# Optimization experiments

Hardware: AMD Instinct MI355X
Metric: run time of the kernel (lower is better)

## Reference

```python
import jax, jax.numpy as jnp
import numpy as np

N_SAMPLES = 32768
N_ATOMS = 1024
ATOM_LEN = 2048
N_TO_KEEP = 1024


def fft_convolve(a, b):
    """Linear convolution via FFT: zero-pad both to 2n, multiply spectra, truncate to n."""
    n = a.shape[-1]
    a = jnp.pad(a, [(0, 0)] * (a.ndim - 1) + [(0, n)])
    b = jnp.pad(b, [(0, 0)] * (b.ndim - 1) + [(0, n)])
    spec = jnp.fft.rfft(a, axis=-1) * jnp.fft.rfft(b, axis=-1)  # broadcast (B,1024,2n//2+1)
    return jnp.fft.irfft(spec, axis=-1)[..., :n]


def sparsify(x, n_to_keep):
    """Keep the top-k raw values over the flattened per-batch feature map; zero the rest."""
    shp = x.shape
    flat = x.reshape(shp[0], -1)                       # (B, 1024*32768)
    vals, idx = jax.lax.top_k(flat, n_to_keep)         # (B, k)
    out = jnp.zeros_like(flat).at[jnp.arange(shp[0])[:, None], idx].set(vals)
    return out.reshape(shp)


def setup_inputs() -> dict:
    key = jax.random.key(0)
    k1, k2 = jax.random.split(key)
    x = jax.random.normal(k1, (2, 1, N_SAMPLES), dtype=jnp.float32)
    # atoms initialized uniform(-0.01, 0.01) in the original module
    atoms = jax.random.uniform(k2, (1, N_ATOMS, ATOM_LEN), dtype=jnp.float32,
                               minval=-0.01, maxval=0.01)
    return {"x": x, "atoms": atoms}


def reference(x, atoms):
    padded = jnp.pad(atoms, ((0, 0), (0, 0), (0, N_SAMPLES - atoms.shape[-1])))  # (1,1024,32768)
    fm = fft_convolve(x, padded)            # (B, 1024, 32768)
    fm = sparsify(fm, N_TO_KEEP)
    recon = fft_convolve(fm, padded)        # (B, 1024, 32768)
    recon = jnp.sum(recon, axis=1, keepdims=True)  # (B, 1, 32768)
    return recon
```

## Files before the change

### kernel.cpp

```cpp
#include <hip/hip_runtime.h>
#include <hip/hip_bf16.h>

#define NS    32768
#define NA    1024
#define AL    2048
#define KKEEP 1024
#define CAPC  (512*1024)

struct Cand { float v; unsigned idx; };

typedef short  short8  __attribute__((ext_vector_type(8)));
typedef short  short4v __attribute__((ext_vector_type(4)));
typedef float  f32x4   __attribute__((ext_vector_type(4)));


__device__ inline unsigned short f2bf(float f) {
    union { float f; unsigned u; } v; v.f = f;
    unsigned r = v.u + 0x7fffu + ((v.u >> 16) & 1u);
    return (unsigned short)(r >> 16);
}

__global__ void prep_kernel(const float* __restrict__ x, const float* __restrict__ atoms,
                            float* __restrict__ psum, unsigned* __restrict__ candCnt,
                            unsigned short* __restrict__ ab16) {
    __shared__ float red[12];
    const int bid = blockIdx.x;
    const int tid = threadIdx.x;
    const int i   = bid * 256 + tid;
    float4 f = *(const float4*)(atoms + (size_t)i * 4);
    ushort4 o;
    o.x = f2bf(f.x); o.y = f2bf(f.y); o.z = f2bf(f.z); o.w = f2bf(f.w);
    *(ushort4*)(ab16 + (size_t)i * 4) = o;
    float sa  = f.x*f.x + f.y*f.y + f.z*f.z + f.w*f.w;
    float sx0 = 0.f, sx1 = 0.f;
    if (i < 16384) {
        float4 xv = *(const float4*)(x + (size_t)i * 4);
        float s = xv.x*xv.x + xv.y*xv.y + xv.z*xv.z + xv.w*xv.w;
        if (i < 8192) sx0 = s; else sx1 = s;
    }
    #pragma unroll
    for (int off = 32; off >= 1; off >>= 1) {
        sa  += __shfl_down(sa , off);
        sx0 += __shfl_down(sx0, off);
        sx1 += __shfl_down(sx1, off);
    }
    if ((tid & 63) == 0) {
        red[(tid >> 6) * 3 + 0] = sa;
        red[(tid >> 6) * 3 + 1] = sx0;
        red[(tid >> 6) * 3 + 2] = sx1;
    }
    __syncthreads();
    if (tid == 0) {
        psum[bid * 3 + 0] = red[0] + red[3] + red[6] + red[9];
        psum[bid * 3 + 1] = red[1] + red[4] + red[7] + red[10];
        psum[bid * 3 + 2] = red[2] + red[5] + red[8] + red[11];
        if (bid == 0) { candCnt[0] = 0u; candCnt[1] = 0u; }
    }
}

#define XRW      2175
#define XRSTRIDE 2192
#define XRB      4384
#define NCPY     4
#define SA_BUF   16384

__device__ inline void gload_lds16(const unsigned short* g, unsigned char* lds) {
    __builtin_amdgcn_global_load_lds((const __attribute__((address_space(1))) void*)g,
                                     (__attribute__((address_space(3))) void*)lds,
                                     16, 0, 0);
}

__global__ __launch_bounds__(256, 3)
void fm_kernel(const float* __restrict__ x, const float* __restrict__ af32,
               const unsigned short* __restrict__ ab16,
               const float* __restrict__ psum, unsigned* __restrict__ candCnt,
               Cand* __restrict__ cand, unsigned cap)
{
    __shared__ __align__(16) unsigned char  sA[2 * SA_BUF];
    __shared__ __align__(16) unsigned short sXR[NCPY * XRSTRIDE];
    __shared__ float    sred[12];
    __shared__ double   sredd[4];
    __shared__ unsigned bq_pos[64];
    __shared__ unsigned bq_idx[64];
    __shared__ int      bq_n;

    const int bid = blockIdx.x;
    const int b   = bid >> 11;
    const int rem = bid & 2047;
    const int a0  = (rem >> 8) * 128;
    const int t0  = (rem & 255) * 128;

    const int tid  = threadIdx.x;
    const int lane = tid & 63;
    const int wid  = tid >> 6;
    const int wm   = wid >> 1;
    const int wn   = wid & 1;
    const int g    = lane >> 4;
    const int ln   = lane & 15;

    const int rot = (bid * 5) & 31;

    const float* __restrict__ xb = x + b * NS;

    for (int ti = tid; ti < XRW; ti += 256) {
        int t = t0 - 2047 + ti;
        float f = (t >= 0) ? xb[t] : 0.f;
        unsigned short h = f2bf(f);
        int p0 = 2174 - ti;
        #pragma unroll
        for (int m = 0; m < NCPY; ++m) sXR[m * XRSTRIDE + p0 + m] = h;
    }

    if (tid == 0) bq_n = 0;
    {
        float pa = 0.f, p0s = 0.f, p1s = 0.f;
        for (int j = tid; j < 2048; j += 256) {
            pa  += psum[3 * j + 0];
            p0s += psum[3 * j + 1];
            p1s += psum[3 * j + 2];
        }
        #pragma unroll
        for (int o = 32; o >= 1; o >>= 1) {
            pa  += __shfl_down(pa , o);
            p0s += __shfl_down(p0s, o);
            p1s += __shfl_down(p1s, o);
        }
        if ((tid & 63) == 0) {
            sred[(tid >> 6) * 3 + 0] = pa;
            sred[(tid >> 6) * 3 + 1] = p0s;
            sred[(tid >> 6) * 3 + 2] = p1s;
        }
    }

    #define STAGE(bf, ck) do {                                                   \
        int kcs = (ck) * 64;                                                     \
        _Pragma("unroll")                                                        \
        for (int it = 0; it < 4; ++it) {                                         \
            int slot = (wid * 4 + it) * 64 + lane;                               \
            int row  = slot >> 3;                                                \
            int blk  = slot & 7;                                                 \
            const unsigned short* gsrc =                                         \
                ab16 + (size_t)(a0 + row) * AL + kcs + ((blk ^ (row & 7)) << 3); \
            gload_lds16(gsrc, sA + (bf) * SA_BUF + (size_t)(wid * 4 + it) * 1024); \
        }                                                                        \
    } while (0)

    f32x4 acc[4][4];
    #pragma unroll
    for (int i = 0; i < 4; ++i)
        #pragma unroll
        for (int j = 0; j < 4; ++j) acc[i][j] = (f32x4)0.0f;

    const int Rbase = 127 - wn * 64 - ln + 8 * g;
    const unsigned char* xrb = (const unsigned char*)sXR;

    int rowoff[4];
    #pragma unroll
    for (int mi = 0; mi < 4; ++mi) rowoff[mi] = (wm * 64 + mi * 16 + ln) * 128;
    const int swz0 = ((0 * 4 + g) ^ (ln & 7)) << 4;
    const int swz1 = ((1 * 4 + g) ^ (ln & 7)) << 4;

    #define LOADB(Rv, dst) do {                                                 \
        int p_ = ((Rv) + 3) & ~3;                                               \
        const unsigned char* a_ =                                               \
            xrb + (unsigned)(p_ - (Rv)) * XRB + (unsigned)p_ * 2u;              \
        short4v lo_ = *(const short4v*)a_;                                      \
        short4v hi_ = *(const short4v*)(a_ + 8);                                \
        dst = __builtin_shufflevector(lo_, hi_, 0, 1, 2, 3, 4, 5, 6, 7);        \
    } while (0)

    short8 b0, b1, b2, b3;

    #define LOADB4(Sv) do {                        \
        LOADB(Rbase      + 32 * (Sv), b0);         \
        LOADB(Rbase - 16 + 32 * (Sv), b1);         \
        LOADB(Rbase - 32 + 32 * (Sv), b2);         \
        LOADB(Rbase - 48 + 32 * (Sv), b3);         \
    } while (0)

    #define ROLLB(Sv) do {                         \
        b3 = b1; b2 = b0;                          \
        LOADB(Rbase      + 32 * (Sv), b0);         \
        LOADB(Rbase - 16 + 32 * (Sv), b1);         \
    } while (0)

    #define MFMAS(mi) do {                                                                  \
        acc[mi][0] = __builtin_amdgcn_mfma_f32_16x16x32_bf16(af[mi], b0, acc[mi][0],0,0,0); \
        acc[mi][1] = __builtin_amdgcn_mfma_f32_16x16x32_bf16(af[mi], b1, acc[mi][1],0,0,0); \
        acc[mi][2] = __builtin_amdgcn_mfma_f32_16x16x32_bf16(af[mi], b2, acc[mi][2],0,0,0); \
        acc[mi][3] = __builtin_amdgcn_mfma_f32_16x16x32_bf16(af[mi], b3, acc[mi][3],0,0,0); \
    } while (0)

    __syncthreads();

    const float SAs = sred[0] + sred[3] + sred[6] + sred[9];
    const float S0s = sred[1] + sred[4] + sred[7] + sred[10];
    const float S1s = sred[2] + sred[5] + sred[8] + sred[11];
    const float sig = sqrtf((SAs * (1.0f / (float)NA)) *
                            (((b == 0) ? S0s : S1s) * (1.0f / (float)NS)));
    const float T0 = 3.70f * sig;
    const float TB = 3.85f * sig;

    LOADB4(rot * 2);

    STAGE(0, rot);
    STAGE(1, (rot + 1) & 31);

    for (int c = 0; c < 32; ++c) {
        const int chunk  = (c + rot) & 31;
        const int nchunk = (c + 1 + rot) & 31;
        const int cur    = c & 1;

        asm volatile("s_waitcnt vmcnt(4)" ::: "memory");
        __builtin_amdgcn_sched_barrier(0);
        __builtin_amdgcn_s_barrier();
        __builtin_amdgcn_sched_barrier(0);

        #pragma unroll
        for (int s = 0; s < 2; ++s) {
            short8 af[4];
            const int soff = cur * SA_BUF + (s ? swz1 : swz0);
            #pragma unroll
            for (int mi = 0; mi < 4; ++mi)
                af[mi] = *(const short8*)(sA + soff + rowoff[mi]);

            __builtin_amdgcn_s_setprio(1);
            MFMAS(0); MFMAS(1); MFMAS(2); MFMAS(3);
            __builtin_amdgcn_s_setprio(0);

            if (s == 0) {
                ROLLB(chunk * 2 + 1);
            } else {
                if (nchunk == 0) { LOADB4(0); }
                else             { ROLLB(nchunk * 2); }
            }
        }

        __builtin_amdgcn_sched_barrier(0);
        __builtin_amdgcn_s_barrier();
        __builtin_amdgcn_sched_barrier(0);

        STAGE(cur, (c + 2 + rot) & 31);
    }
    #undef LOADB
    #undef LOADB4
    #undef ROLLB
    #undef MFMAS
    #undef STAGE

    #pragma unroll
    for (int mi = 0; mi < 4; ++mi) {
        #pragma unroll
        for (int ni = 0; ni < 4; ++ni) {
            #pragma unroll
            for (int r = 0; r < 4; ++r) {
                float v = acc[mi][ni][r];
                if (v > T0) {
                    unsigned a = (unsigned)(a0 + wm * 64 + mi * 16 + g * 4 + r);
                    unsigned t = (unsigned)(t0 + wn * 64 + ni * 16 + ln);
                    unsigned idx = (a << 15) | t;
                    unsigned pos = atomicAdd(&candCnt[b], 1u);
                    if (pos < cap) {
                        Cand cc; cc.v = v; cc.idx = idx;
                        cand[(size_t)b * cap + pos] = cc;
                        if (v > TB) {
                            int q = atomicAdd(&bq_n, 1);
                            if (q < 64) { bq_pos[q] = pos; bq_idx[q] = idx; }
                        }
                    }
                }
            }
        }
    }
    __syncthreads();

    int nq = bq_n; if (nq > 64) nq = 64;
    for (int e = 0; e < nq; ++e) {
        const unsigned ie = bq_idx[e];
        const unsigned pe = bq_pos[e];
        const int aa = (int)(ie >> 15);
        const int tt = (int)(ie & (NS - 1));
        const float* __restrict__ ar = af32 + (size_t)aa * AL;
        double s = 0.0;
        #pragma unroll
        for (int kk = 0; kk < 8; ++kk) {
            int k = tid + kk * 256;
            int xi = tt - k;
            if (xi >= 0) s += (double)ar[k] * (double)xb[xi];
        }
        #pragma unroll
        for (int o = 32; o >= 1; o >>= 1) s += __shfl_down(s, o);
        if (lane == 0) sredd[wid] = s;
        __syncthreads();
        if (tid == 0)
            cand[(size_t)b * cap + pe].v =
                (float)(sredd[0] + sredd[1] + sredd[2] + sredd[3]);
        __syncthreads();
    }
}

#define SELCAP 16384

__global__ void select_kernel(const unsigned* __restrict__ candCnt,
                              const Cand* __restrict__ cand, Cand* __restrict__ sel,
                              unsigned cap) {
    __shared__ float    s_vals[SELCAP];
    __shared__ float    s_red[16];
    __shared__ int      s_cnt;
    __shared__ int      s_nA;
    __shared__ int      s_nT;
    __shared__ int      s_exact;
    __shared__ float    s_tau;
    __shared__ Cand     s_A[KKEEP];
    __shared__ unsigned s_T[256];

    const int b = blockIdx.x;
    const Cand* __restrict__ cb = cand + (size_t)b * cap;
    const int n   = (int)min(candCnt[b], cap);
    const int tid = threadIdx.x;

    if (n <= KKEEP) {
        for (int i = tid; i < KKEEP; i += blockDim.x) {
            Cand z; z.v = 0.f; z.idx = 0u;
            sel[b * KKEEP + i] = (i < n) ? cb[i] : z;
        }
        return;
    }

    const bool useLds = (n <= SELCAP);
    if (useLds)
        for (int i = tid; i < n; i += blockDim.x) s_vals[i] = cb[i].v;

    float m = 0.f;
    if (useLds) { __syncthreads();
        for (int i = tid; i < n; i += blockDim.x) m = fmaxf(m, s_vals[i]);
    } else {
        for (int i = tid; i < n; i += blockDim.x) m = fmaxf(m, cb[i].v);
    }
    #pragma unroll
    for (int o = 32; o >= 1; o >>= 1) m = fmaxf(m, __shfl_down(m, o));
    if ((tid & 63) == 0) s_red[tid >> 6] = m;
    if (tid == 0) s_exact = 0;
    __syncthreads();
    float hi;
    {
        float mm = 0.f;
        #pragma unroll
        for (int w = 0; w < 16; ++w) mm = fmaxf(mm, s_red[w]);
        hi = mm;
    }
    float lo = 0.f;
    for (int iter = 0; iter < 64; ++iter) {
        float mid = 0.5f * (lo + hi);
        if (!(mid > lo && mid < hi)) break;
        if (tid == 0) s_cnt = 0;
        __syncthreads();
        int c = 0;
        if (useLds) for (int i = tid; i < n; i += blockDim.x) c += (s_vals[i] > mid) ? 1 : 0;
        else        for (int i = tid; i < n; i += blockDim.x) c += (cb[i].v  > mid) ? 1 : 0;
        #pragma unroll
        for (int o = 32; o >= 1; o >>= 1) c += __shfl_down(c, o);
        if ((tid & 63) == 0) atomicAdd(&s_cnt, c);
        __syncthreads();
        int cm = s_cnt;
        __syncthreads();
        if (cm == KKEEP) { if (tid == 0) { s_tau = mid; s_exact = 1; } break; }
        if (cm > KKEEP) lo = mid; else hi = mid;
    }
    __syncthreads();

    const int   exact = s_exact;
    const float tau   = exact ? s_tau : hi;

    for (int i = tid; i < KKEEP; i += blockDim.x) { s_A[i].v = 0.f; s_A[i].idx = 0u; }
    if (tid == 0) { s_nA = 0; s_nT = 0; }
    __syncthreads();

    for (int i = tid; i < n; i += blockDim.x) {
        float v = cb[i].v;
        if (v > tau) {
            int p = atomicAdd(&s_nA, 1);
            if (p < KKEEP) s_A[p] = cb[i];
        } else if (!exact && v == tau) {
            int p = atomicAdd(&s_nT, 1);
            if (p < 256) s_T[p] = cb[i].idx;
        }
    }
    __syncthreads();
    if (tid == 0) {
        int nA = s_nA; if (nA > KKEEP) nA = KKEEP;
        int need = KKEEP - nA;
        int nT = s_nT; if (nT > 256) nT = 256;
        for (int r = 0; r < need && r < nT; ++r) {
            unsigned best = 0xffffffffu; int bj = -1;
            for (int j = 0; j < nT; ++j) if (s_T[j] < best) { best = s_T[j]; bj = j; }
            Cand c; c.v = tau; c.idx = best;
            s_A[nA + r] = c;
            if (bj >= 0) s_T[bj] = 0xffffffffu;
        }
    }
    __syncthreads();
    for (int i = tid; i < KKEEP; i += blockDim.x) sel[b * KKEEP + i] = s_A[i];
}

__global__ void recon_kernel(const float* __restrict__ atoms, const Cand* __restrict__ sel,
                             float* __restrict__ out) {
    __shared__ float s_cv[KKEEP];
    __shared__ int   s_ca[KKEEP];
    __shared__ int   s_ct[KKEEP];
    __shared__ int   s_n;
    const int b    = blockIdx.x >> 7;
    const int tseg = (blockIdx.x & 127) << 8;
    const int t    = tseg + threadIdx.x;
    if (threadIdx.x == 0) s_n = 0;
    __syncthreads();
    for (int i = threadIdx.x; i < KKEEP; i += blockDim.x) {
        Cand c = sel[b * KKEEP + i];
        int t0e = (int)(c.idx & (NS - 1));
        if (c.v != 0.f && t0e <= tseg + 255 && t0e + (AL - 1) >= tseg) {
            int p = atomicAdd(&s_n, 1);
            s_cv[p] = c.v;
            s_ca[p] = (int)(c.idx >> 15);
            s_ct[p] = t0e;
        }
    }
    __syncthreads();
    const int n = s_n;
    float acc = 0.f;
    for (int e = 0; e < n; ++e) {
        int d = t - s_ct[e];
        if ((unsigned)d < (unsigned)AL)
            acc += s_cv[e] * atoms[(size_t)s_ca[e] * AL + d];
    }
    out[b * NS + t] = acc;
}

extern "C" void kernel_launch(void* const* d_in, const int* in_sizes, int n_in,
                              void* d_out, int out_size, void* d_ws, size_t ws_size,
                              hipStream_t stream) {
    const float* x     = (const float*)d_in[0];
    const float* atoms = (const float*)d_in[1];
    float* out = (float*)d_out;

    unsigned*       candCnt = (unsigned*)d_ws;
    float*          psum    = (float*)((char*)d_ws + 64);
    Cand*           sel     = (Cand*)((char*)d_ws + 32768);
    unsigned short* ab16    = (unsigned short*)((char*)d_ws + 65536);
    const size_t    candOff = 65536 + (size_t)NA * AL * 2;
    Cand*           cand    = (Cand*)((char*)d_ws + candOff);

    unsigned cap = CAPC;
    if (ws_size > candOff + 2 * sizeof(Cand) * 1024) {
        size_t fit = (ws_size - candOff) / (2 * sizeof(Cand));
        if (fit < cap) cap = (unsigned)fit;
    } else {
        cap = 1024;
    }

    prep_kernel  <<<2048, 256, 0, stream>>>(x, atoms, psum, candCnt, ab16);
    fm_kernel    <<<2 * (NA / 128) * (NS / 128), 256, 0, stream>>>(x, atoms, ab16, psum, candCnt, cand, cap);
    select_kernel<<<2, 1024, 0, stream>>>(candCnt, cand, sel, cap);
    recon_kernel <<<256, 256, 0, stream>>>(atoms, sel, out);
}
```

Measured before the change: 420.4 us.

## Move fp64 band refinement out of fm_kernel into separate wave-per-candidate kernel

The exact fp64 recomputation of borderline candidates (value above a higher band threshold) is taken out of the GEMM-style fm_kernel, where it ran serially per block with two block barriers per candidate. A new refine_band kernel scans all candidates after fm_kernel, and one wavefront refines each candidate above the band threshold. This removes tail latency and LDS from the hot kernel, which may help occupancy, and spreads the refinement across the whole GPU. The cost is an extra launch and a full re-read of the candidate list. The 64-per-block cap on refined candidates is also gone.

```diff
diff --git a/kernel.cpp b/kernel.cpp
--- a/kernel.cpp
+++ b/kernel.cpp
@@ -71,18 +71,14 @@
 }
 
 __global__ __launch_bounds__(256, 3)
-void fm_kernel(const float* __restrict__ x, const float* __restrict__ af32,
+void fm_kernel(const float* __restrict__ x,
                const unsigned short* __restrict__ ab16,
                const float* __restrict__ psum, unsigned* __restrict__ candCnt,
                Cand* __restrict__ cand, unsigned cap)
 {
     __shared__ __align__(16) unsigned char  sA[2 * SA_BUF];
     __shared__ __align__(16) unsigned short sXR[NCPY * XRSTRIDE];
-    __shared__ float    sred[12];
-    __shared__ double   sredd[4];
-    __shared__ unsigned bq_pos[64];
-    __shared__ unsigned bq_idx[64];
-    __shared__ int      bq_n;
+    __shared__ float sred[12];
 
     const int bid = blockIdx.x;
     const int b   = bid >> 11;
@@ -111,7 +107,6 @@
         for (int m = 0; m < NCPY; ++m) sXR[m * XRSTRIDE + p0 + m] = h;
     }
 
-    if (tid == 0) bq_n = 0;
     {
         float pa = 0.f, p0s = 0.f, p1s = 0.f;
         for (int j = tid; j < 2048; j += 256) {
@@ -199,7 +194,6 @@
     const float sig = sqrtf((SAs * (1.0f / (float)NA)) *
                             (((b == 0) ? S0s : S1s) * (1.0f / (float)NS)));
     const float T0 = 3.70f * sig;
-    const float TB = 3.85f * sig;
 
     LOADB4(rot * 2);
 
@@ -263,39 +257,70 @@
                     if (pos < cap) {
                         Cand cc; cc.v = v; cc.idx = idx;
                         cand[(size_t)b * cap + pos] = cc;
-                        if (v > TB) {
-                            int q = atomicAdd(&bq_n, 1);
-                            if (q < 64) { bq_pos[q] = pos; bq_idx[q] = idx; }
-                        }
                     }
                 }
             }
         }
     }
-    __syncthreads();
-
-    int nq = bq_n; if (nq > 64) nq = 64;
-    for (int e = 0; e < nq; ++e) {
-        const unsigned ie = bq_idx[e];
-        const unsigned pe = bq_pos[e];
-        const int aa = (int)(ie >> 15);
-        const int tt = (int)(ie & (NS - 1));
-        const float* __restrict__ ar = af32 + (size_t)aa * AL;
+}
+
+__global__ void refine_band(const float* __restrict__ x, const float* __restrict__ atoms,
+                            const float* __restrict__ psum,
+                            const unsigned* __restrict__ candCnt, Cand* __restrict__ cand,
+                            unsigned cap) {
+    __shared__ float sred[12];
+    const int tid  = threadIdx.x;
+    const int lane = tid & 63;
+
+    {
+        float pa = 0.f, p0s = 0.f, p1s = 0.f;
+        for (int j = tid; j < 2048; j += 256) {
+            pa  += psum[3 * j + 0];
+            p0s += psum[3 * j + 1];
+            p1s += psum[3 * j + 2];
+        }
+        #pragma unroll
+        for (int o = 32; o >= 1; o >>= 1) {
+            pa  += __shfl_down(pa , o);
+            p0s += __shfl_down(p0s, o);
+            p1s += __shfl_down(p1s, o);
+        }
+        if ((tid & 63) == 0) {
+            sred[(tid >> 6) * 3 + 0] = pa;
+            sred[(tid >> 6) * 3 + 1] = p0s;
+            sred[(tid >> 6) * 3 + 2] = p1s;
+        }
+    }
+    __syncthreads();
+    const float SAs = sred[0] + sred[3] + sred[6] + sred[9];
+    const float S0s = sred[1] + sred[4] + sred[7] + sred[10];
+    const float S1s = sred[2] + sred[5] + sred[8] + sred[11];
+    const float TB0 = 3.85f * sqrtf((SAs * (1.0f / (float)NA)) * (S0s * (1.0f / (float)NS)));
+    const float TB1 = 3.85f * sqrtf((SAs * (1.0f / (float)NA)) * (S1s * (1.0f / (float)NS)));
+
+    const int wv = (int)((blockIdx.x * blockDim.x + threadIdx.x) >> 6);
+    const int nw = (int)((gridDim.x * blockDim.x) >> 6);
+    const int n0 = (int)min(candCnt[0], cap);
+    const int n1 = (int)min(candCnt[1], cap);
+    const int total = n0 + n1;
+    for (int c = wv; c < total; c += nw) {
+        const int b = (c < n0) ? 0 : 1;
+        const size_t ci = (c < n0) ? (size_t)c : ((size_t)cap + (size_t)(c - n0));
+        const Cand cc = cand[ci];
+        if (cc.v <= ((b == 0) ? TB0 : TB1)) continue;
+        const unsigned idx = cc.idx;
+        const int a = (int)(idx >> 15);
+        const int t = (int)(idx & (NS - 1));
+        const float* __restrict__ ar = atoms + (size_t)a * AL;
+        const float* __restrict__ xr = x + b * NS;
         double s = 0.0;
-        #pragma unroll
-        for (int kk = 0; kk < 8; ++kk) {
-            int k = tid + kk * 256;
-            int xi = tt - k;
-            if (xi >= 0) s += (double)ar[k] * (double)xb[xi];
+        for (int k = lane; k < AL; k += 64) {
+            int xi = t - k;
+            if (xi >= 0) s += (double)ar[k] * (double)xr[xi];
         }
         #pragma unroll
         for (int o = 32; o >= 1; o >>= 1) s += __shfl_down(s, o);
-        if (lane == 0) sredd[wid] = s;
-        __syncthreads();
-        if (tid == 0)
-            cand[(size_t)b * cap + pe].v =
-                (float)(sredd[0] + sredd[1] + sredd[2] + sredd[3]);
-        __syncthreads();
+        if (lane == 0) cand[ci].v = (float)s;
     }
 }
 
@@ -458,7 +483,8 @@
     }
 
     prep_kernel  <<<2048, 256, 0, stream>>>(x, atoms, psum, candCnt, ab16);
-    fm_kernel    <<<2 * (NA / 128) * (NS / 128), 256, 0, stream>>>(x, atoms, ab16, psum, candCnt, cand, cap);
+    fm_kernel    <<<2 * (NA / 128) * (NS / 128), 256, 0, stream>>>(x, ab16, psum, candCnt, cand, cap);
+    refine_band  <<<512, 256, 0, stream>>>(x, atoms, psum, candCnt, cand, cap);
     select_kernel<<<2, 1024, 0, stream>>>(candCnt, cand, sel, cap);
     recon_kernel <<<256, 256, 0, stream>>>(atoms, sel, out);
 }
```

After: 414.8 us. About the same (-1.3%).
